# Kernel optimization log

Hardware: AMD Instinct MI355X
Metric: run time of the kernel (lower is better)

Reference implementation:

```python
import jax, jax.numpy as jnp
import numpy as np

B, S, D, H, L, OUT = 64, 512, 256, 512, 2, 128


def setup_inputs() -> dict:
    key = jax.random.key(0)
    ks = jax.random.split(key, 11)
    s = 0.04  # ~1/sqrt(H) init scale, avoids gate saturation
    return {
        "x": jax.random.normal(ks[0], (B, S, D), jnp.float32),
        "W_ih0": jax.random.normal(ks[1], (4 * H, D), jnp.float32) * s,
        "W_hh0": jax.random.normal(ks[2], (4 * H, H), jnp.float32) * s,
        "b_ih0": jax.random.normal(ks[3], (4 * H,), jnp.float32) * s,
        "b_hh0": jax.random.normal(ks[4], (4 * H,), jnp.float32) * s,
        "W_ih1": jax.random.normal(ks[5], (4 * H, H), jnp.float32) * s,
        "W_hh1": jax.random.normal(ks[6], (4 * H, H), jnp.float32) * s,
        "b_ih1": jax.random.normal(ks[7], (4 * H,), jnp.float32) * s,
        "b_hh1": jax.random.normal(ks[8], (4 * H,), jnp.float32) * s,
        "fc_w": jax.random.normal(ks[9], (OUT, H), jnp.float32) * s,
        "fc_b": jax.random.normal(ks[10], (OUT,), jnp.float32) * s,
    }


def _lstm_layer(x_sbd, W_ih, W_hh, b_ih, b_hh):
    # x_sbd: [S, B, Din]. Precompute input contribution to all gates (one big GEMM).
    xg = jnp.einsum("sbd,gd->sbg", x_sbd, W_ih) + b_ih + b_hh  # [S, B, 4H]
    Hd = W_hh.shape[1]
    h0 = jnp.zeros((x_sbd.shape[1], Hd), x_sbd.dtype)
    c0 = jnp.zeros_like(h0)

    def step(carry, xg_t):
        h, c = carry
        gates = xg_t + h @ W_hh.T  # [B, 4H]
        i, f, g, o = jnp.split(gates, 4, axis=-1)  # PyTorch gate order i,f,g,o
        i, f, o = jax.nn.sigmoid(i), jax.nn.sigmoid(f), jax.nn.sigmoid(o)
        g = jnp.tanh(g)
        c = f * c + i * g
        h = o * jnp.tanh(c)
        return (h, c), h

    (_, _), hs = jax.lax.scan(step, (h0, c0), xg)
    return hs  # [S, B, H]


def reference(x, W_ih0, W_hh0, b_ih0, b_hh0, W_ih1, W_hh1, b_ih1, b_hh1, fc_w, fc_b):
    xs = jnp.transpose(x, (1, 0, 2))  # [S, B, D], time-major for scan
    h1 = _lstm_layer(xs, W_ih0, W_hh0, b_ih0, b_hh0)
    h2 = _lstm_layer(h1, W_ih1, W_hh1, b_ih1, b_hh1)
    last = h2[-1]  # [B, H] == out[:, -1, :]
    return last @ fc_w.T + fc_b  # [B, OUT]
```

## Files before the change

kernel.cpp:

```cpp
#include <hip/hip_runtime.h>

typedef unsigned long long u64;
typedef unsigned int u32;
typedef __attribute__((ext_vector_type(8))) short short8;
typedef __attribute__((ext_vector_type(4))) float floatx4;

#define Bc   64
#define Sc   512
#define Dc   256
#define Hc   512
#define OUTc 128

#define NWG  256
#define NTHR 512
#define NL0  128
#define JPW  16
#define NRW  64
#define KPB  1032

#define HQ   8192
#define WS_BYTES (4096 + 5 * HQ * 8)

__device__ __forceinline__ u64 cload8(const u64* p) {
    return __hip_atomic_load(p, __ATOMIC_RELAXED, __HIP_MEMORY_SCOPE_AGENT);
}
__device__ __forceinline__ void cstore4(u32* p, u32 v) {
    __hip_atomic_store(p, v, __ATOMIC_RELAXED, __HIP_MEMORY_SCOPE_AGENT);
}

__device__ __forceinline__ short bf16_rne(float f) {
    u32 u = __float_as_uint(f);
    u += 0x7fffu + ((u >> 16) & 1u);
    return (short)(u >> 16);
}
__device__ __forceinline__ float4 unpack4(u64 v) {
    u32 lo = (u32)v, hi = (u32)(v >> 32);
    float4 f;
    f.x = __uint_as_float(lo << 16);
    f.y = __uint_as_float(lo & 0xffff0000u);
    f.z = __uint_as_float(hi << 16);
    f.w = __uint_as_float(hi & 0xffff0000u);
    return f;
}
__device__ __forceinline__ u32 pack2_rne(float a, float b) {
    u32 ua = __float_as_uint(a), ub = __float_as_uint(b);
    ua += 0x7fffu + ((ua >> 16) & 1u);
    ub += 0x7fffu + ((ub >> 16) & 1u);
    return (ua >> 16) | (ub & 0xffff0000u);
}
__device__ __forceinline__ short8 frag2(u64 a, u64 b) {
    union { u64 u[2]; short8 s; } c; c.u[0] = a; c.u[1] = b; return c.s;
}

__device__ __forceinline__ void wait32(const u32* fbase, u32 target, int lane) {
    const u32* p = fbase + (lane & 31);
    for (;;) {
        u32 f = __hip_atomic_load(p, __ATOMIC_RELAXED, __HIP_MEMORY_SCOPE_AGENT);
        if (__all(f >= target)) return;
        __builtin_amdgcn_s_sleep(8);
    }
}
__device__ __forceinline__ void wait128(const u32* flags, u32 target, int lane) {
    const u32* p0 = flags + lane; const u32* p1 = flags + lane + 64;
    for (;;) {
        u32 f0 = __hip_atomic_load(p0, __ATOMIC_RELAXED, __HIP_MEMORY_SCOPE_AGENT);
        u32 f1 = __hip_atomic_load(p1, __ATOMIC_RELAXED, __HIP_MEMORY_SCOPE_AGENT);
        if (__all((f0 >= target) && (f1 >= target))) return;
        __builtin_amdgcn_s_sleep(8);
    }
}

__device__ __forceinline__ float sigmoidf_fast(float v) {
    return 1.0f / (1.0f + __expf(-v));
}
__device__ __forceinline__ float tanhf_fast(float v) {
    return 2.0f / (1.0f + __expf(-2.0f * v)) - 1.0f;
}

extern "C" __global__ void __launch_bounds__(NTHR)
lstm_persist(const float* __restrict__ x,
             const float* __restrict__ Wih0, const float* __restrict__ Whh0,
             const float* __restrict__ bih0, const float* __restrict__ bhh0,
             const float* __restrict__ Wih1, const float* __restrict__ Whh1,
             const float* __restrict__ bih1, const float* __restrict__ bhh1,
             const float* __restrict__ fcw, const float* __restrict__ fcb,
             float* __restrict__ out, float* __restrict__ wsf)
{
    __shared__ short Wl[NRW * KPB];
    __shared__ float red[2 * 4 * 16 * 20];

    u32* flags0 = (u32*)wsf;
    u32* flags1 = flags0 + 128;
    u64* h1b = (u64*)((char*)wsf + 4096);
    u64* h2b = h1b + 3 * HQ;

    const int wg  = blockIdx.x;
    const int tid = threadIdx.x;
    const bool isL1 = (wg >= NL0);
    const int wgl = isL1 ? wg - NL0 : wg;
    const int rg = wgl >> 2, bg = wgl & 3;
    const int j0 = rg * JPW;
    const int K  = isL1 ? 1024 : 768;
    const int KD = isL1 ? 512  : 256;

    {
        const float* Wi = isL1 ? Wih1 : Wih0;
        const float* Wh = isL1 ? Whh1 : Whh0;
        for (int r = 0; r < NRW; ++r) {
            const int row = (r >> 4) * Hc + j0 + (r & 15);
            for (int c = tid; c < K; c += NTHR) {
                float v = (c < KD) ? Wi[(size_t)row * KD + c] : Wh[(size_t)row * Hc + (c - KD)];
                Wl[r * KPB + c] = bf16_rne(v);
            }
        }
    }
    __syncthreads();

    const int w    = tid >> 6;
    const int lane = tid & 63;
    const int g    = w >> 1;
    const int half = w & 1;
    const int quad = lane >> 4;
    const int c16  = lane & 15;
    const int bglob = bg * 16 + c16;
    const int wrowb = (g * 16 + c16) * KPB;

    const int bl = tid & 15, jp = tid >> 4;
    float cst[2] = {0.0f, 0.0f};
    float bias2[2][4];
    {
        const float* bi = isL1 ? bih1 : bih0;
        const float* bh = isL1 ? bhh1 : bhh0;
#pragma unroll
        for (int jj2 = 0; jj2 < 2; ++jj2) {
            const int j = j0 + 2 * jp + jj2;
#pragma unroll
            for (int gg = 0; gg < 4; ++gg)
                bias2[jj2][gg] = bi[gg * Hc + j] + bh[gg * Hc + j];
        }
    }
    const int hsoff = ((j0 + 2 * jp) >> 2) * 128 + 2 * (bg * 16 + bl) + (jp & 1);

    u32* myflag = (isL1 ? flags1 : flags0) + bg * 32 + rg;
    const u32* f0b = flags0 + bg * 32;
    const u32* f1b = flags1 + bg * 32;

    for (int s = 0; s < Sc; ++s) {
        floatx4 acc = {0.0f, 0.0f, 0.0f, 0.0f};

        auto mfma_h = [&](int wk0, int hk0, int nblk, const u64* hb_) {
            u64 F[16];
#pragma unroll
            for (int i = 0; i < 8; ++i) {
                if (i >= nblk) break;
                const int q8 = (hk0 >> 2) + i * 8 + quad * 2;
                F[2 * i]     = cload8(hb_ + (size_t)q8 * 64 + bglob);
                F[2 * i + 1] = cload8(hb_ + (size_t)(q8 + 1) * 64 + bglob);
            }
#pragma unroll
            for (int i = 0; i < 8; ++i) {
                if (i >= nblk) break;
                short8 A = *(const short8*)&Wl[wrowb + wk0 + i * 32 + quad * 8];
                short8 Bv = frag2(F[2 * i], F[2 * i + 1]);
                acc = __builtin_amdgcn_mfma_f32_16x16x32_bf16(A, Bv, acc, 0, 0, 0);
            }
        };

        const int mW = s % 3;
        const int mR = (s + 2) % 3;

        if (!isL1) {
            {
                const float* xp = x + (size_t)bglob * Sc * Dc + (size_t)s * Dc
                                + half * 128 + quad * 8;
                float Xv[32];
#pragma unroll
                for (int i = 0; i < 8; ++i)
                    *(float4*)&Xv[4 * i] = *(const float4*)(xp + (i >> 1) * 32 + (i & 1) * 4);
#pragma unroll
                for (int i = 0; i < 4; ++i) {
                    short8 Bv;
#pragma unroll
                    for (int j = 0; j < 8; ++j) Bv[j] = bf16_rne(Xv[i * 8 + j]);
                    short8 A = *(const short8*)&Wl[wrowb + half * 128 + i * 32 + quad * 8];
                    acc = __builtin_amdgcn_mfma_f32_16x16x32_bf16(A, Bv, acc, 0, 0, 0);
                }
            }
            if (w == 0) {
                wait32(f0b, (u32)s, lane);
                wait32(f1b, (u32)(s >= 3 ? s - 2 : 0), lane);
            }
            __syncthreads();
            mfma_h(256 + half * 256, half * 256, 8, h1b + (size_t)mR * HQ);
        } else {
            if (w == 0) wait32(f1b, (u32)s, lane);
            __syncthreads();
            mfma_h(512 + half * 256, half * 256, 8, h2b + (size_t)((s + 1) & 1) * HQ);
            if (w == 0) wait32(f0b, (u32)(s + 1), lane);
            __syncthreads();
            mfma_h(half * 256, half * 256, 8, h1b + (size_t)mW * HQ);
        }

        *(float4*)&red[((half * 4 + g) * 16 + c16) * 20 + quad * 4] =
            make_float4(acc[0], acc[1], acc[2], acc[3]);
        __syncthreads();

        if (tid < 128) {
            float hv[2];
#pragma unroll
            for (int jj2 = 0; jj2 < 2; ++jj2) {
                const int jl = 2 * jp + jj2;
                float gv[4];
#pragma unroll
                for (int gg = 0; gg < 4; ++gg)
                    gv[gg] = red[((0 + gg) * 16 + bl) * 20 + jl]
                           + red[((4 + gg) * 16 + bl) * 20 + jl] + bias2[jj2][gg];
                const float ig = sigmoidf_fast(gv[0]);
                const float fg = sigmoidf_fast(gv[1]);
                const float gt = tanhf_fast(gv[2]);
                const float og = sigmoidf_fast(gv[3]);
                cst[jj2] = fg * cst[jj2] + ig * gt;
                hv[jj2] = og * tanhf_fast(cst[jj2]);
            }
            u64* hb = isL1 ? (h2b + (size_t)(s & 1) * HQ)
                           : (h1b + (size_t)mW * HQ);
            cstore4((u32*)hb + hsoff, pack2_rne(hv[0], hv[1]));
        }
        __syncthreads();
        if (tid == 0)
            __hip_atomic_store(myflag, (u32)(s + 1), __ATOMIC_RELAXED, __HIP_MEMORY_SCOPE_AGENT);
    }

    if (wg < Bc) {
        if (w == 0) wait128(flags1, (u32)Sc, lane);
        __syncthreads();
        const int b = wg;
        const u64* h2 = h2b + (size_t)((Sc - 1) & 1) * HQ;
        const int o = tid & 127, q = tid >> 7;
        const float* wrow = fcw + (size_t)o * Hc;
        float a = 0.0f;
        for (int k4 = q * 32; k4 < q * 32 + 32; ++k4) {
            const float4 f = unpack4(cload8(h2 + (size_t)k4 * 64 + b));
            const float* wr = wrow + 4 * k4;
            a += f.x * wr[0] + f.y * wr[1] + f.z * wr[2] + f.w * wr[3];
        }
        __syncthreads();
        red[q * 128 + o] = a;
        __syncthreads();
        if (tid < OUTc)
            out[b * OUTc + tid] = red[tid] + red[128 + tid] + red[256 + tid] + red[384 + tid] + fcb[tid];
    }
}

extern "C" void kernel_launch(void* const* d_in, const int* in_sizes, int n_in,
                              void* d_out, int out_size, void* d_ws, size_t ws_size,
                              hipStream_t stream) {
    const float* x    = (const float*)d_in[0];
    const float* Wih0 = (const float*)d_in[1];
    const float* Whh0 = (const float*)d_in[2];
    const float* bih0 = (const float*)d_in[3];
    const float* bhh0 = (const float*)d_in[4];
    const float* Wih1 = (const float*)d_in[5];
    const float* Whh1 = (const float*)d_in[6];
    const float* bih1 = (const float*)d_in[7];
    const float* bhh1 = (const float*)d_in[8];
    const float* fcw  = (const float*)d_in[9];
    const float* fcb  = (const float*)d_in[10];
    float* out = (float*)d_out;
    float* wsf = (float*)d_ws;

    hipMemsetAsync(d_ws, 0, WS_BYTES, stream);

    lstm_persist<<<dim3(NWG), dim3(NTHR), 0, stream>>>(
        x, Wih0, Whh0, bih0, bhh0, Wih1, Whh1, bih1, bhh1, fcw, fcb, out, wsf);
}
```

Before: 2.163 ms.

## Merge layer-1 flag waits into one barrier and shorten spin-wait sleep

Spin-wait loops now sleep for 1 unit instead of 8, so workgroups see flag updates sooner. The two separate flag waits in layer 0 become one combined poll. In layer 1, the wait for its own previous step and the wait for layer 0's current output are merged into a single wait and barrier, and all h loads are issued before the MFMAs. This removes one __syncthreads per step and lets layer-1 recurrent work overlap less with the layer-0 dependency, but it means layer 1 can no longer start its own recurrent MFMAs before layer 0 finishes; the tighter polling also adds memory traffic.

Result: faster. 2.037 ms (-5.8%).

```diff
diff --git a/kernel.cpp b/kernel.cpp
--- a/kernel.cpp
+++ b/kernel.cpp
@@ -57,7 +57,17 @@
     for (;;) {
         u32 f = __hip_atomic_load(p, __ATOMIC_RELAXED, __HIP_MEMORY_SCOPE_AGENT);
         if (__all(f >= target)) return;
-        __builtin_amdgcn_s_sleep(8);
+        __builtin_amdgcn_s_sleep(1);
+    }
+}
+__device__ __forceinline__ void wait2(const u32* fa, u32 ta, const u32* fb, u32 tb, int lane) {
+    const u32* pa = fa + (lane & 31);
+    const u32* pb = fb + (lane & 31);
+    for (;;) {
+        u32 va = __hip_atomic_load(pa, __ATOMIC_RELAXED, __HIP_MEMORY_SCOPE_AGENT);
+        u32 vb = __hip_atomic_load(pb, __ATOMIC_RELAXED, __HIP_MEMORY_SCOPE_AGENT);
+        if (__all((va >= ta) && (vb >= tb))) return;
+        __builtin_amdgcn_s_sleep(1);
     }
 }
 __device__ __forceinline__ void wait128(const u32* flags, u32 target, int lane) {
@@ -66,7 +76,7 @@
         u32 f0 = __hip_atomic_load(p0, __ATOMIC_RELAXED, __HIP_MEMORY_SCOPE_AGENT);
         u32 f1 = __hip_atomic_load(p1, __ATOMIC_RELAXED, __HIP_MEMORY_SCOPE_AGENT);
         if (__all((f0 >= target) && (f1 >= target))) return;
-        __builtin_amdgcn_s_sleep(8);
+        __builtin_amdgcn_s_sleep(1);
     }
 }
 
@@ -148,24 +158,6 @@
     for (int s = 0; s < Sc; ++s) {
         floatx4 acc = {0.0f, 0.0f, 0.0f, 0.0f};
 
-        auto mfma_h = [&](int wk0, int hk0, int nblk, const u64* hb_) {
-            u64 F[16];
-#pragma unroll
-            for (int i = 0; i < 8; ++i) {
-                if (i >= nblk) break;
-                const int q8 = (hk0 >> 2) + i * 8 + quad * 2;
-                F[2 * i]     = cload8(hb_ + (size_t)q8 * 64 + bglob);
-                F[2 * i + 1] = cload8(hb_ + (size_t)(q8 + 1) * 64 + bglob);
-            }
-#pragma unroll
-            for (int i = 0; i < 8; ++i) {
-                if (i >= nblk) break;
-                short8 A = *(const short8*)&Wl[wrowb + wk0 + i * 32 + quad * 8];
-                short8 Bv = frag2(F[2 * i], F[2 * i + 1]);
-                acc = __builtin_amdgcn_mfma_f32_16x16x32_bf16(A, Bv, acc, 0, 0, 0);
-            }
-        };
-
         const int mW = s % 3;
         const int mR = (s + 2) % 3;
 
@@ -186,19 +178,53 @@
                     acc = __builtin_amdgcn_mfma_f32_16x16x32_bf16(A, Bv, acc, 0, 0, 0);
                 }
             }
-            if (w == 0) {
-                wait32(f0b, (u32)s, lane);
-                wait32(f1b, (u32)(s >= 3 ? s - 2 : 0), lane);
-            }
+            if (w == 0) wait2(f0b, (u32)s, f1b, (u32)(s >= 3 ? s - 2 : 0), lane);
             __syncthreads();
-            mfma_h(256 + half * 256, half * 256, 8, h1b + (size_t)mR * HQ);
+            {
+                const u64* hb_ = h1b + (size_t)mR * HQ;
+                u64 F[16];
+#pragma unroll
+                for (int i = 0; i < 8; ++i) {
+                    const int q8 = (half * 64) + i * 8 + quad * 2;
+                    F[2 * i]     = cload8(hb_ + (size_t)q8 * 64 + bglob);
+                    F[2 * i + 1] = cload8(hb_ + (size_t)(q8 + 1) * 64 + bglob);
+                }
+#pragma unroll
+                for (int i = 0; i < 8; ++i) {
+                    short8 A = *(const short8*)&Wl[wrowb + 256 + half * 256 + i * 32 + quad * 8];
+                    acc = __builtin_amdgcn_mfma_f32_16x16x32_bf16(A, frag2(F[2 * i], F[2 * i + 1]), acc, 0, 0, 0);
+                }
+            }
         } else {
-            if (w == 0) wait32(f1b, (u32)s, lane);
+            if (w == 0) wait2(f1b, (u32)s, f0b, (u32)(s + 1), lane);
             __syncthreads();
-            mfma_h(512 + half * 256, half * 256, 8, h2b + (size_t)((s + 1) & 1) * HQ);
-            if (w == 0) wait32(f0b, (u32)(s + 1), lane);
-            __syncthreads();
-            mfma_h(half * 256, half * 256, 8, h1b + (size_t)mW * HQ);
+            {
+                const u64* hb2 = h2b + (size_t)((s + 1) & 1) * HQ;
+                const u64* hb1 = h1b + (size_t)mW * HQ;
+                u64 F[32];
+#pragma unroll
+                for (int i = 0; i < 8; ++i) {
+                    const int q8 = (half * 64) + i * 8 + quad * 2;
+                    F[2 * i]     = cload8(hb2 + (size_t)q8 * 64 + bglob);
+                    F[2 * i + 1] = cload8(hb2 + (size_t)(q8 + 1) * 64 + bglob);
+                }
+#pragma unroll
+                for (int i = 0; i < 8; ++i) {
+                    const int q8 = (half * 64) + i * 8 + quad * 2;
+                    F[16 + 2 * i] = cload8(hb1 + (size_t)q8 * 64 + bglob);
+                    F[17 + 2 * i] = cload8(hb1 + (size_t)(q8 + 1) * 64 + bglob);
+                }
+#pragma unroll
+                for (int i = 0; i < 8; ++i) {
+                    short8 A = *(const short8*)&Wl[wrowb + 512 + half * 256 + i * 32 + quad * 8];
+                    acc = __builtin_amdgcn_mfma_f32_16x16x32_bf16(A, frag2(F[2 * i], F[2 * i + 1]), acc, 0, 0, 0);
+                }
+#pragma unroll
+                for (int i = 0; i < 8; ++i) {
+                    short8 A = *(const short8*)&Wl[wrowb + half * 256 + i * 32 + quad * 8];
+                    acc = __builtin_amdgcn_mfma_f32_16x16x32_bf16(A, frag2(F[16 + 2 * i], F[17 + 2 * i]), acc, 0, 0, 0);
+                }
+            }
         }
 
         *(float4*)&red[((half * 4 + g) * 16 + c16) * 20 + quad * 4] =
```
